# Kernel tuning notes

Hardware: AMD Instinct MI355X
Metric: run time of the kernel (lower is better)

## Reference

```python
import jax, jax.numpy as jnp
import numpy as np
from functools import partial

D_MODEL = 256
D_STATE = 16
DT_RANK = 16  # ceil(d_model/16)
LN_EPS = 1e-5


def setup_inputs() -> dict:
    key = jax.random.key(0)
    ks = jax.random.split(key, 8)
    B, L, d, N, r = 16, 2048, D_MODEL, D_STATE, DT_RANK
    x = jax.random.normal(ks[0], (B, L, d), dtype=jnp.float32)
    # LayerNorm params
    ln_w = jnp.ones((d,), jnp.float32)
    ln_b = jnp.zeros((d,), jnp.float32)
    # S6 params
    x_proj_w = jax.random.normal(ks[1], (d, r + 2 * N), jnp.float32) / np.sqrt(d)
    dt_proj_w = jax.random.normal(ks[2], (r, d), jnp.float32) / np.sqrt(r)
    dt_proj_b = jax.random.uniform(ks[3], (d,), jnp.float32, -4.0, -2.0)  # softplus -> small dt
    A_log = jnp.log(jnp.tile(jnp.arange(1, N + 1, dtype=jnp.float32), (d, 1)))  # (d, N)
    D_skip = jnp.ones((d,), jnp.float32)
    # GLU params
    glu_w = jax.random.normal(ks[4], (d, 2 * d), jnp.float32) / np.sqrt(d)
    glu_b = jnp.zeros((2 * d,), jnp.float32)
    return {"x": x, "ln_w": ln_w, "ln_b": ln_b, "x_proj_w": x_proj_w,
            "dt_proj_w": dt_proj_w, "dt_proj_b": dt_proj_b, "A_log": A_log,
            "D_skip": D_skip, "glu_w": glu_w, "glu_b": glu_b}


def _layernorm(x, w, b):
    mu = jnp.mean(x, -1, keepdims=True)
    var = jnp.mean(jnp.square(x - mu), -1, keepdims=True)
    return (x - mu) * jax.lax.rsqrt(var + LN_EPS) * w + b


def _s6(x, x_proj_w, dt_proj_w, dt_proj_b, A_log, D_skip):
    # x: (B, L, d) selective scan (S6)
    Bsz, L, d = x.shape
    N = A_log.shape[1]
    A = -jnp.exp(A_log)                       # (d, N)
    dbl = x @ x_proj_w                        # (B, L, r+2N)
    dt, Bm, Cm = jnp.split(dbl, [DT_RANK, DT_RANK + N], axis=-1)
    delta = jax.nn.softplus(dt @ dt_proj_w + dt_proj_b)  # (B, L, d)

    def step(h, inp):
        d_t, b_t, c_t, x_t = inp              # (B,d),(B,N),(B,N),(B,d)
        dA = jnp.exp(d_t[..., None] * A)      # (B, d, N)
        h = dA * h + (d_t * x_t)[..., None] * b_t[:, None, :]
        y = jnp.einsum('bdn,bn->bd', h, c_t)
        return h, y

    h0 = jnp.zeros((Bsz, d, N), x.dtype)
    xs = (jnp.swapaxes(delta, 0, 1), jnp.swapaxes(Bm, 0, 1),
          jnp.swapaxes(Cm, 0, 1), jnp.swapaxes(x, 0, 1))
    _, ys = jax.lax.scan(step, h0, xs)        # ys: (L, B, d)
    return jnp.swapaxes(ys, 0, 1) + x * D_skip


def _glu(x, w, b):
    d = x.shape[-1]
    out = x @ w + b
    return out[..., :d] * jax.nn.sigmoid(out[..., d:])


@jax.jit
def reference(x, ln_w, ln_b, x_proj_w, dt_proj_w, dt_proj_b, A_log, D_skip, glu_w, glu_b):
    skip = x
    h = _layernorm(x, ln_w, ln_b)
    h = _s6(h, x_proj_w, dt_proj_w, dt_proj_b, A_log, D_skip)
    h = jax.nn.gelu(h, approximate=False)     # dropout = identity (eval)
    h = _glu(h, glu_w, glu_b)
    return h + skip
```

## Files before the change

### kernel.cpp

```cpp
#include <hip/hip_runtime.h>
#include <hip/hip_bf16.h>

#define BB 16
#define LL 2048
#define DD 256
#define NN 16
#define RR 16
#define CH 64
#define LC (LL/CH)

static __device__ __forceinline__ float bf2f(unsigned short u) {
    return __uint_as_float(((unsigned)u) << 16);
}
static __device__ __forceinline__ unsigned short f2bf(float f) {
    unsigned u = __float_as_uint(f);
    u += 0x7FFFu + ((u >> 16) & 1u);
    return (unsigned short)(u >> 16);
}

typedef __attribute__((ext_vector_type(8))) short bf16x8;
typedef __attribute__((ext_vector_type(4))) short bf16x4;
typedef __attribute__((ext_vector_type(4))) float f32x4;

static __device__ __forceinline__ void pow_tree(float E, float* e) {
    e[0] = E;
    e[1] = E * E;
    e[2] = e[1] * E;
    e[3] = e[1] * e[1];
    e[4] = e[3] * e[0];  e[5] = e[3] * e[1];  e[6] = e[3] * e[2];  e[7] = e[3] * e[3];
    e[8] = e[7] * e[0];  e[9] = e[7] * e[1];  e[10] = e[7] * e[2]; e[11] = e[7] * e[3];
    e[12] = e[7] * e[4]; e[13] = e[7] * e[5]; e[14] = e[7] * e[6]; e[15] = e[7] * e[7];
}

__global__ __launch_bounds__(256) void k_prep_wx(
    const float* __restrict__ xw, unsigned short* __restrict__ Wxt)
{
    const int idx = blockIdx.x * 256 + threadIdx.x;
    const int n  = idx >> 6;
    const int k0 = (idx & 63) * 4;
    #pragma unroll
    for (int i = 0; i < 4; ++i) {
        float v = (n < 48) ? xw[(size_t)(k0 + i) * 48 + n] : 0.f;
        Wxt[(size_t)n * DD + k0 + i] = f2bf(v);
    }
}

__global__ __launch_bounds__(256) void k_transpose(
    const float* __restrict__ W, unsigned short* __restrict__ Wt)
{
    __shared__ unsigned short s[32][33];
    const int bx = blockIdx.x;
    const int by = blockIdx.y;
    const int t = threadIdx.x;
    const int r = t >> 5, cc = t & 31;
    #pragma unroll
    for (int i = 0; i < 4; ++i)
        s[r + 8*i][cc] = f2bf(W[(size_t)(by*32 + r + 8*i)*512 + bx*32 + cc]);
    __syncthreads();
    #pragma unroll
    for (int i = 0; i < 4; ++i)
        Wt[(size_t)(bx*32 + r + 8*i)*256 + by*32 + cc] = s[cc][r + 8*i];
}

__global__ __launch_bounds__(256) void k_ln_fused(
    const float* __restrict__ x,
    const float* __restrict__ ln_w,
    const float* __restrict__ ln_b,
    const unsigned short* __restrict__ Wxt,
    const float* __restrict__ dtw,
    const float* __restrict__ dtb,
    unsigned short* __restrict__ xln,
    unsigned short* __restrict__ delta,
    float* __restrict__ Bv,
    float* __restrict__ Cv)
{
    const int t = threadIdx.x;
    const int m0 = blockIdx.x * 32;
    const int row = t >> 3, seg = t & 7;
    const int grow = m0 + row;

    __shared__ unsigned short As[32][264];
    __shared__ float sdt[32][20];
    __shared__ float sdtw[16*256];
    __shared__ float slnw[256], slnb[256], sdtb[256];

    {
        const int tt = t & 63;
        if (t < 64)       *(float4*)&slnw[tt*4] = *(const float4*)&ln_w[tt*4];
        else if (t < 128) *(float4*)&slnb[tt*4] = *(const float4*)&ln_b[tt*4];
        else if (t < 192) *(float4*)&sdtb[tt*4] = *(const float4*)&dtb[tt*4];
        #pragma unroll
        for (int k = 0; k < 4; ++k)
            *(float4*)&sdtw[(k*256 + t)*4] = *(const float4*)&dtw[(k*256 + t)*4];
    }

    float v[32];
    #pragma unroll
    for (int i = 0; i < 8; ++i)
        *(float4*)&v[i*4] = *(const float4*)(x + (size_t)grow*DD + i*32 + seg*4);

    float s = 0.f, q = 0.f;
    #pragma unroll
    for (int i = 0; i < 32; ++i) { s += v[i]; q = fmaf(v[i], v[i], q); }
    #pragma unroll
    for (int o = 1; o < 8; o <<= 1) {
        s += __shfl_xor(s, o);
        q += __shfl_xor(q, o);
    }
    const float mu = s * (1.f/DD);
    const float rs = rsqrtf(q * (1.f/DD) - mu*mu + 1e-5f);
    __syncthreads();

    unsigned short o16[32];
    #pragma unroll
    for (int i = 0; i < 8; ++i) {
        const int c = i*32 + seg*4;
        const float4 wv = *(const float4*)&slnw[c];
        const float4 bv = *(const float4*)&slnb[c];
        o16[i*4+0] = f2bf((v[i*4+0]-mu)*rs*wv.x + bv.x);
        o16[i*4+1] = f2bf((v[i*4+1]-mu)*rs*wv.y + bv.y);
        o16[i*4+2] = f2bf((v[i*4+2]-mu)*rs*wv.z + bv.z);
        o16[i*4+3] = f2bf((v[i*4+3]-mu)*rs*wv.w + bv.w);
    }
    #pragma unroll
    for (int i = 0; i < 8; ++i) {
        const int c = i*32 + seg*4;
        *(bf16x4*)&xln[(size_t)grow*DD + c] = *(bf16x4*)&o16[i*4];
        *(bf16x4*)&As[row][c]               = *(bf16x4*)&o16[i*4];
    }
    __syncthreads();

    const int w = t >> 6, lane = t & 63;
    const int cl = lane & 15, rq = lane >> 4;
    const int mh = (w & 1) * 16;
    const int nh = (w >> 1) * 32;
    f32x4 acc0 = {0.f,0.f,0.f,0.f}, acc1 = {0.f,0.f,0.f,0.f};
    #pragma unroll
    for (int k0 = 0; k0 < 256; k0 += 32) {
        const bf16x8 a  = *(const bf16x8*)&As[mh + cl][k0 + rq*8];
        const bf16x8 b0 = *(const bf16x8*)&Wxt[(size_t)(nh + cl)*DD + k0 + rq*8];
        acc0 = __builtin_amdgcn_mfma_f32_16x16x32_bf16(a, b0, acc0, 0, 0, 0);
        if (w < 2) {
            const bf16x8 b1 = *(const bf16x8*)&Wxt[(size_t)(nh + 16 + cl)*DD + k0 + rq*8];
            acc1 = __builtin_amdgcn_mfma_f32_16x16x32_bf16(a, b1, acc1, 0, 0, 0);
        }
    }
    if (w < 2) {
        #pragma unroll
        for (int r = 0; r < 4; ++r) {
            sdt[mh + rq*4 + r][cl] = acc0[r];
            Bv[(size_t)(m0 + mh + rq*4 + r)*NN + cl] = acc1[r];
        }
    } else {
        #pragma unroll
        for (int r = 0; r < 4; ++r)
            Cv[(size_t)(m0 + mh + rq*4 + r)*NN + cl] = acc0[r];
    }
    __syncthreads();

    float dt[16];
    #pragma unroll
    for (int j = 0; j < 16; ++j) dt[j] = sdt[row][j];
    #pragma unroll
    for (int i = 0; i < 8; ++i) {
        const int c = i*32 + seg*4;
        float4 a4 = *(const float4*)&sdtb[c];
        #pragma unroll
        for (int j = 0; j < 16; ++j) {
            const float4 w4 = *(const float4*)&sdtw[j*256 + c];
            a4.x = fmaf(dt[j], w4.x, a4.x);
            a4.y = fmaf(dt[j], w4.y, a4.y);
            a4.z = fmaf(dt[j], w4.z, a4.z);
            a4.w = fmaf(dt[j], w4.w, a4.w);
        }
        unsigned short d16[4];
        #pragma unroll
        for (int jj = 0; jj < 4; ++jj) {
            const float ac = (&a4.x)[jj];
            const float sp = (ac > 15.f) ? ac
                : 0.69314718f * log2f(1.f + exp2f(ac * 1.44269504f));
            d16[jj] = f2bf(sp);
        }
        *(bf16x4*)&delta[(size_t)grow*DD + c] = *(bf16x4*)&d16[0];
    }
}

template<bool FAST>
__device__ __forceinline__ void scan1_impl(
    const unsigned short* __restrict__ delta,
    const unsigned short* __restrict__ xln,
    const float (*sB)[16],
    const float* al, int b, int c, int d,
    float* h, float* dsum)
{
    const int l0 = c * LC;
    for (int l = 0; l < LC; ++l) {
        const size_t base = (size_t)b*LL + l0 + l;
        const float dl = bf2f(delta[base*DD + d]);
        const float xl = bf2f(xln[base*DD + d]);
        const float dx = dl * xl;
        *dsum += dl;
        float e[NN];
        if (FAST) pow_tree(exp2f(al[0]*dl), e);
        else {
            #pragma unroll
            for (int n = 0; n < NN; ++n) e[n] = exp2f(al[n]*dl);
        }
        #pragma unroll
        for (int n = 0; n < NN; ++n)
            h[n] = fmaf(e[n], h[n], dx * sB[l][n]);
    }
}

__global__ __launch_bounds__(256) void k_scan1(
    const unsigned short* __restrict__ delta,
    const unsigned short* __restrict__ xln,
    const float* __restrict__ Bv,
    const float* __restrict__ A_log,
    float* __restrict__ S, float* __restrict__ Dsum)
{
    const int blk = blockIdx.x;
    const int c = blk & (CH-1);
    const int b = blk >> 6;
    const int d = threadIdx.x;
    __shared__ float sB[LC][16];
    if (d < 128) {
        const int l = d >> 2, q = (d & 3) * 4;
        *(float4*)&sB[l][q] = *(const float4*)&Bv[((size_t)b*LL + c*LC + l)*NN + q];
    }
    float al[NN];
    bool fast = true;
    #pragma unroll
    for (int n = 0; n < NN; ++n) {
        al[n] = -expf(A_log[d*NN + n]) * 1.44269504f;
        fast = fast && (fabsf(al[n] - (n+1)*al[0]) <= 1e-3f*fabsf(al[n]) + 1e-6f);
    }
    float h[NN];
    #pragma unroll
    for (int n = 0; n < NN; ++n) h[n] = 0.f;
    float dsum = 0.f;
    __syncthreads();
    if (fast) scan1_impl<true >(delta, xln, sB, al, b, c, d, h, &dsum);
    else      scan1_impl<false>(delta, xln, sB, al, b, c, d, h, &dsum);
    const size_t o = (size_t)blk * NN * DD + d;
    #pragma unroll
    for (int n = 0; n < NN; ++n) S[o + n*DD] = h[n];
    Dsum[(size_t)blk*DD + d] = dsum;
}

__global__ __launch_bounds__(256) void k_combine(
    const float* __restrict__ S, const float* __restrict__ Dsum,
    const float* __restrict__ A_log, float* __restrict__ Hin)
{
    const int idx = blockIdx.x * 256 + threadIdx.x;
    const int d = idx & 255;
    const int n = (idx >> 8) & 15;
    const int b = idx >> 12;
    const float al = -expf(A_log[d*NN + n]) * 1.44269504f;
    float h = 0.f;
    for (int c = 0; c < CH; ++c) {
        const size_t blk = (size_t)b*CH + c;
        const size_t o = blk*NN*DD + (size_t)n*DD + d;
        Hin[o] = h;
        h = fmaf(exp2f(al * Dsum[blk*DD + d]), h, S[o]);
    }
}

template<bool FAST>
__device__ __forceinline__ void scan2_impl(
    const unsigned short* __restrict__ delta,
    const unsigned short* __restrict__ xln,
    const float (*sB)[16], const float (*sC)[16],
    const float* al, int b, int c, int d,
    float* h, float dsk, unsigned short* __restrict__ g)
{
    const int l0 = c * LC;
    for (int l = 0; l < LC; ++l) {
        const size_t base = (size_t)b*LL + l0 + l;
        const float dl = bf2f(delta[base*DD + d]);
        const float xl = bf2f(xln[base*DD + d]);
        const float dx = dl * xl;
        float e[NN];
        if (FAST) pow_tree(exp2f(al[0]*dl), e);
        else {
            #pragma unroll
            for (int n = 0; n < NN; ++n) e[n] = exp2f(al[n]*dl);
        }
        float y = 0.f;
        #pragma unroll
        for (int n = 0; n < NN; ++n) {
            h[n] = fmaf(e[n], h[n], dx * sB[l][n]);
            y = fmaf(h[n], sC[l][n], y);
        }
        const float vv = y + xl * dsk;
        const float u  = 0.7978845608f * (vv + 0.044715f*vv*vv*vv);
        const float t2 = exp2f(2.8853900818f * u);
        const float th = 1.f - 2.f/(t2 + 1.f);
        g[base*DD + d] = f2bf(0.5f * vv * (1.f + th));
    }
}

__global__ __launch_bounds__(256) void k_scan2(
    const unsigned short* __restrict__ delta,
    const unsigned short* __restrict__ xln,
    const float* __restrict__ Bv,
    const float* __restrict__ Cv,
    const float* __restrict__ A_log,
    const float* __restrict__ Hin,
    const float* __restrict__ Dskip,
    unsigned short* __restrict__ g)
{
    const int blk = blockIdx.x;
    const int c = blk & (CH-1);
    const int b = blk >> 6;
    const int d = threadIdx.x;
    __shared__ float sB[LC][16], sC[LC][16];
    if (d < 128) {
        const int l = d >> 2, q = (d & 3) * 4;
        *(float4*)&sB[l][q] = *(const float4*)&Bv[((size_t)b*LL + c*LC + l)*NN + q];
    } else {
        const int dd = d - 128;
        const int l = dd >> 2, q = (dd & 3) * 4;
        *(float4*)&sC[l][q] = *(const float4*)&Cv[((size_t)b*LL + c*LC + l)*NN + q];
    }
    float al[NN];
    bool fast = true;
    #pragma unroll
    for (int n = 0; n < NN; ++n) {
        al[n] = -expf(A_log[d*NN + n]) * 1.44269504f;
        fast = fast && (fabsf(al[n] - (n+1)*al[0]) <= 1e-3f*fabsf(al[n]) + 1e-6f);
    }
    float h[NN];
    const size_t ob = (size_t)blk * NN * DD + d;
    #pragma unroll
    for (int n = 0; n < NN; ++n) h[n] = Hin[ob + n*DD];
    const float dsk = Dskip[d];
    __syncthreads();
    if (fast) scan2_impl<true >(delta, xln, sB, sC, al, b, c, d, h, dsk, g);
    else      scan2_impl<false>(delta, xln, sB, sC, al, b, c, d, h, dsk, g);
}

__global__ __launch_bounds__(256) void k_glu(
    const unsigned short* __restrict__ g,
    const unsigned short* __restrict__ Wt,
    const float* __restrict__ gb,
    const float* __restrict__ x,
    float* __restrict__ out)
{
    __shared__ unsigned short As[64][40];
    __shared__ unsigned short Bl[64][40];
    __shared__ unsigned short Bh[64][40];
    const int n0 = blockIdx.x * 64;
    const int m0 = blockIdx.y * 64;
    const int t = threadIdx.x;
    const int w = t >> 6, lane = t & 63;
    const int r = t >> 2, q = t & 3;
    const int cl = lane & 15, rq = lane >> 4;
    f32x4 accL[4], accH[4];
    const f32x4 zz = {0.f, 0.f, 0.f, 0.f};
    #pragma unroll
    for (int nf = 0; nf < 4; ++nf) { accL[nf] = zz; accH[nf] = zz; }

    for (int k0 = 0; k0 < 256; k0 += 32) {
        *(bf16x8*)(&As[r][q*8]) = *(const bf16x8*)(&g [(size_t)(m0+r)*DD + k0 + q*8]);
        *(bf16x8*)(&Bl[r][q*8]) = *(const bf16x8*)(&Wt[(size_t)(n0+r)*DD + k0 + q*8]);
        *(bf16x8*)(&Bh[r][q*8]) = *(const bf16x8*)(&Wt[(size_t)(n0+256+r)*DD + k0 + q*8]);
        __syncthreads();
        const bf16x8 a = *(const bf16x8*)(&As[w*16 + cl][rq*8]);
        #pragma unroll
        for (int nf = 0; nf < 4; ++nf) {
            const bf16x8 bl = *(const bf16x8*)(&Bl[nf*16 + cl][rq*8]);
            const bf16x8 bh = *(const bf16x8*)(&Bh[nf*16 + cl][rq*8]);
            accL[nf] = __builtin_amdgcn_mfma_f32_16x16x32_bf16(a, bl, accL[nf], 0, 0, 0);
            accH[nf] = __builtin_amdgcn_mfma_f32_16x16x32_bf16(a, bh, accH[nf], 0, 0, 0);
        }
        __syncthreads();
    }
    #pragma unroll
    for (int nf = 0; nf < 4; ++nf) {
        const int j = n0 + nf*16 + cl;
        const float bL = gb[j];
        const float bH = gb[j + 256];
        #pragma unroll
        for (int rr = 0; rr < 4; ++rr) {
            const int m = m0 + w*16 + rq*4 + rr;
            const float lo = accL[nf][rr] + bL;
            const float hi = accH[nf][rr] + bH;
            const float sg = 1.f / (1.f + exp2f(-1.44269504f * hi));
            out[(size_t)m*DD + j] = lo * sg + x[(size_t)m*DD + j];
        }
    }
}

extern "C" void kernel_launch(void* const* d_in, const int* in_sizes, int n_in,
                              void* d_out, int out_size, void* d_ws, size_t ws_size,
                              hipStream_t stream)
{
    const float* x    = (const float*)d_in[0];
    const float* ln_w = (const float*)d_in[1];
    const float* ln_b = (const float*)d_in[2];
    const float* xpw  = (const float*)d_in[3];
    const float* dtw  = (const float*)d_in[4];
    const float* dtb  = (const float*)d_in[5];
    const float* alog = (const float*)d_in[6];
    const float* dsk  = (const float*)d_in[7];
    const float* gw   = (const float*)d_in[8];
    const float* gb   = (const float*)d_in[9];
    float* out = (float*)d_out;

    char* ws = (char*)d_ws;
    size_t off = 0;
    auto alloc = [&](size_t bytes) {
        char* p = ws + off; off += (bytes + 255) & ~(size_t)255; return p;
    };
    unsigned short* xln   = (unsigned short*)alloc((size_t)BB*LL*DD*2);
    unsigned short* delta = (unsigned short*)alloc((size_t)BB*LL*DD*2);
    float*          Bvp   = (float*)         alloc((size_t)BB*LL*NN*4);
    float*          Cvp   = (float*)         alloc((size_t)BB*LL*NN*4);
    float*          S     = (float*)         alloc((size_t)BB*CH*NN*DD*4);
    float*          Dsum  = (float*)         alloc((size_t)BB*CH*DD*4);
    float*          Hin   = (float*)         alloc((size_t)BB*CH*NN*DD*4);
    unsigned short* Wt    = (unsigned short*)alloc((size_t)512*256*2);
    unsigned short* Wxt   = (unsigned short*)alloc((size_t)64*256*2);
    unsigned short* g     = delta;

    k_prep_wx<<<16, 256, 0, stream>>>(xpw, Wxt);
    k_transpose<<<dim3(16, 8), 256, 0, stream>>>(gw, Wt);
    k_ln_fused<<<1024, 256, 0, stream>>>(x, ln_w, ln_b, Wxt, dtw, dtb, xln, delta, Bvp, Cvp);
    k_scan1<<<BB*CH, 256, 0, stream>>>(delta, xln, Bvp, alog, S, Dsum);
    k_combine<<<256, 256, 0, stream>>>(S, Dsum, alog, Hin);
    k_scan2<<<BB*CH, 256, 0, stream>>>(delta, xln, Bvp, Cvp, alog, Hin, dsk, g);
    k_glu<<<dim3(4, 512), 256, 0, stream>>>(g, Wt, gb, x, out);
}
```

Baseline: 117.3 us.

## Fuse GLU matmul into scan2 via shared-memory activations; batch combine loads

The second scan pass now writes its GELU outputs for each 32-row chunk into shared memory, and the same block runs the GLU MFMA matmul, sigmoid gate and residual add directly. This removes the bf16 g buffer round trip through global memory and one kernel launch. Each block now reads the full 512x256 transposed GLU weight straight from global memory, with no LDS tiling, so the weights are re-read by all 1024 blocks and mostly served from cache. The combine kernel is remapped to one block per (batch, state) and prefetches 8 chunk values at a time to expose memory-level parallelism.

```diff
diff --git a/kernel.cpp b/kernel.cpp
--- a/kernel.cpp
+++ b/kernel.cpp
@@ -252,17 +252,26 @@
     const float* __restrict__ S, const float* __restrict__ Dsum,
     const float* __restrict__ A_log, float* __restrict__ Hin)
 {
-    const int idx = blockIdx.x * 256 + threadIdx.x;
-    const int d = idx & 255;
-    const int n = (idx >> 8) & 15;
-    const int b = idx >> 12;
+    const int bi = blockIdx.x;
+    const int d = threadIdx.x;
+    const int n = bi & 15;
+    const int b = bi >> 4;
     const float al = -expf(A_log[d*NN + n]) * 1.44269504f;
     float h = 0.f;
-    for (int c = 0; c < CH; ++c) {
-        const size_t blk = (size_t)b*CH + c;
-        const size_t o = blk*NN*DD + (size_t)n*DD + d;
-        Hin[o] = h;
-        h = fmaf(exp2f(al * Dsum[blk*DD + d]), h, S[o]);
+    for (int c0 = 0; c0 < CH; c0 += 8) {
+        float ds8[8], s8[8];
+        #pragma unroll
+        for (int i = 0; i < 8; ++i) {
+            const size_t blk = (size_t)b*CH + c0 + i;
+            ds8[i] = Dsum[blk*DD + d];
+            s8[i]  = S[(blk*NN + n)*DD + d];
+        }
+        #pragma unroll
+        for (int i = 0; i < 8; ++i) {
+            const size_t blk = (size_t)b*CH + c0 + i;
+            Hin[(blk*NN + n)*DD + d] = h;
+            h = fmaf(exp2f(al * ds8[i]), h, s8[i]);
+        }
     }
 }
 
@@ -271,8 +280,9 @@
     const unsigned short* __restrict__ delta,
     const unsigned short* __restrict__ xln,
     const float (*sB)[16], const float (*sC)[16],
+    unsigned short (*gs)[264],
     const float* al, int b, int c, int d,
-    float* h, float dsk, unsigned short* __restrict__ g)
+    float* h, float dsk)
 {
     const int l0 = c * LC;
     for (int l = 0; l < LC; ++l) {
@@ -296,11 +306,11 @@
         const float u  = 0.7978845608f * (vv + 0.044715f*vv*vv*vv);
         const float t2 = exp2f(2.8853900818f * u);
         const float th = 1.f - 2.f/(t2 + 1.f);
-        g[base*DD + d] = f2bf(0.5f * vv * (1.f + th));
-    }
-}
-
-__global__ __launch_bounds__(256) void k_scan2(
+        gs[l][d] = f2bf(0.5f * vv * (1.f + th));
+    }
+}
+
+__global__ __launch_bounds__(256) void k_scan2glu(
     const unsigned short* __restrict__ delta,
     const unsigned short* __restrict__ xln,
     const float* __restrict__ Bv,
@@ -308,13 +318,18 @@
     const float* __restrict__ A_log,
     const float* __restrict__ Hin,
     const float* __restrict__ Dskip,
-    unsigned short* __restrict__ g)
+    const unsigned short* __restrict__ Wt,
+    const float* __restrict__ gb,
+    const float* __restrict__ x,
+    float* __restrict__ out)
 {
     const int blk = blockIdx.x;
     const int c = blk & (CH-1);
     const int b = blk >> 6;
     const int d = threadIdx.x;
     __shared__ float sB[LC][16], sC[LC][16];
+    __shared__ unsigned short gs[LC][264];
+
     if (d < 128) {
         const int l = d >> 2, q = (d & 3) * 4;
         *(float4*)&sB[l][q] = *(const float4*)&Bv[((size_t)b*LL + c*LC + l)*NN + q];
@@ -336,58 +351,57 @@
     for (int n = 0; n < NN; ++n) h[n] = Hin[ob + n*DD];
     const float dsk = Dskip[d];
     __syncthreads();
-    if (fast) scan2_impl<true >(delta, xln, sB, sC, al, b, c, d, h, dsk, g);
-    else      scan2_impl<false>(delta, xln, sB, sC, al, b, c, d, h, dsk, g);
-}
-
-__global__ __launch_bounds__(256) void k_glu(
-    const unsigned short* __restrict__ g,
-    const unsigned short* __restrict__ Wt,
-    const float* __restrict__ gb,
-    const float* __restrict__ x,
-    float* __restrict__ out)
-{
-    __shared__ unsigned short As[64][40];
-    __shared__ unsigned short Bl[64][40];
-    __shared__ unsigned short Bh[64][40];
-    const int n0 = blockIdx.x * 64;
-    const int m0 = blockIdx.y * 64;
-    const int t = threadIdx.x;
-    const int w = t >> 6, lane = t & 63;
-    const int r = t >> 2, q = t & 3;
+    if (fast) scan2_impl<true >(delta, xln, sB, sC, gs, al, b, c, d, h, dsk);
+    else      scan2_impl<false>(delta, xln, sB, sC, gs, al, b, c, d, h, dsk);
+    __syncthreads();
+
+    const int w = d >> 6, lane = d & 63;
     const int cl = lane & 15, rq = lane >> 4;
-    f32x4 accL[4], accH[4];
-    const f32x4 zz = {0.f, 0.f, 0.f, 0.f};
-    #pragma unroll
-    for (int nf = 0; nf < 4; ++nf) { accL[nf] = zz; accH[nf] = zz; }
-
+    f32x4 acc[8];
+    const f32x4 zz = {0.f,0.f,0.f,0.f};
+    #pragma unroll
+    for (int nf = 0; nf < 8; ++nf) acc[nf] = zz;
+    f32x4 acc2[8];
+    #pragma unroll
+    for (int nf = 0; nf < 8; ++nf) acc2[nf] = zz;
+
+    #pragma unroll
     for (int k0 = 0; k0 < 256; k0 += 32) {
-        *(bf16x8*)(&As[r][q*8]) = *(const bf16x8*)(&g [(size_t)(m0+r)*DD + k0 + q*8]);
-        *(bf16x8*)(&Bl[r][q*8]) = *(const bf16x8*)(&Wt[(size_t)(n0+r)*DD + k0 + q*8]);
-        *(bf16x8*)(&Bh[r][q*8]) = *(const bf16x8*)(&Wt[(size_t)(n0+256+r)*DD + k0 + q*8]);
-        __syncthreads();
-        const bf16x8 a = *(const bf16x8*)(&As[w*16 + cl][rq*8]);
-        #pragma unroll
-        for (int nf = 0; nf < 4; ++nf) {
-            const bf16x8 bl = *(const bf16x8*)(&Bl[nf*16 + cl][rq*8]);
-            const bf16x8 bh = *(const bf16x8*)(&Bh[nf*16 + cl][rq*8]);
-            accL[nf] = __builtin_amdgcn_mfma_f32_16x16x32_bf16(a, bl, accL[nf], 0, 0, 0);
-            accH[nf] = __builtin_amdgcn_mfma_f32_16x16x32_bf16(a, bh, accH[nf], 0, 0, 0);
-        }
-        __syncthreads();
-    }
+        const bf16x8 a0 = *(const bf16x8*)&gs[cl][k0 + rq*8];
+        const bf16x8 a1 = *(const bf16x8*)&gs[16 + cl][k0 + rq*8];
+        #pragma unroll
+        for (int nf = 0; nf < 8; ++nf) {
+            const int nrow = (nf < 4) ? (w*64 + nf*16 + cl)
+                                      : (256 + w*64 + (nf-4)*16 + cl);
+            const bf16x8 bfr = *(const bf16x8*)&Wt[(size_t)nrow*DD + k0 + rq*8];
+            acc [nf] = __builtin_amdgcn_mfma_f32_16x16x32_bf16(a0, bfr, acc [nf], 0, 0, 0);
+            acc2[nf] = __builtin_amdgcn_mfma_f32_16x16x32_bf16(a1, bfr, acc2[nf], 0, 0, 0);
+        }
+    }
+    const int l0 = c * LC;
     #pragma unroll
     for (int nf = 0; nf < 4; ++nf) {
-        const int j = n0 + nf*16 + cl;
+        const int j = w*64 + nf*16 + cl;
         const float bL = gb[j];
         const float bH = gb[j + 256];
         #pragma unroll
         for (int rr = 0; rr < 4; ++rr) {
-            const int m = m0 + w*16 + rq*4 + rr;
-            const float lo = accL[nf][rr] + bL;
-            const float hi = accH[nf][rr] + bH;
-            const float sg = 1.f / (1.f + exp2f(-1.44269504f * hi));
-            out[(size_t)m*DD + j] = lo * sg + x[(size_t)m*DD + j];
+            {
+                const int m = rq*4 + rr;
+                const size_t o = ((size_t)b*LL + l0 + m)*DD + j;
+                const float lo = acc[nf][rr] + bL;
+                const float hi = acc[nf+4][rr] + bH;
+                const float sg = 1.f / (1.f + exp2f(-1.44269504f * hi));
+                out[o] = lo * sg + x[o];
+            }
+            {
+                const int m = 16 + rq*4 + rr;
+                const size_t o = ((size_t)b*LL + l0 + m)*DD + j;
+                const float lo = acc2[nf][rr] + bL;
+                const float hi = acc2[nf+4][rr] + bH;
+                const float sg = 1.f / (1.f + exp2f(-1.44269504f * hi));
+                out[o] = lo * sg + x[o];
+            }
         }
     }
 }
@@ -422,13 +436,11 @@
     float*          Hin   = (float*)         alloc((size_t)BB*CH*NN*DD*4);
     unsigned short* Wt    = (unsigned short*)alloc((size_t)512*256*2);
     unsigned short* Wxt   = (unsigned short*)alloc((size_t)64*256*2);
-    unsigned short* g     = delta;
 
     k_prep_wx<<<16, 256, 0, stream>>>(xpw, Wxt);
     k_transpose<<<dim3(16, 8), 256, 0, stream>>>(gw, Wt);
     k_ln_fused<<<1024, 256, 0, stream>>>(x, ln_w, ln_b, Wxt, dtw, dtb, xln, delta, Bvp, Cvp);
     k_scan1<<<BB*CH, 256, 0, stream>>>(delta, xln, Bvp, alog, S, Dsum);
     k_combine<<<256, 256, 0, stream>>>(S, Dsum, alog, Hin);
-    k_scan2<<<BB*CH, 256, 0, stream>>>(delta, xln, Bvp, Cvp, alog, Hin, dsk, g);
-    k_glu<<<dim3(4, 512), 256, 0, stream>>>(g, Wt, gb, x, out);
-}
+    k_scan2glu<<<BB*CH, 256, 0, stream>>>(delta, xln, Bvp, Cvp, alog, Hin, dsk, Wt, gb, x, out);
+}
```

Result: slower. 128.2 us (+9.3%).
